# Performance work log

Hardware: AMD Instinct MI355X
Metric: run time of the kernel (lower is better)

## Reference

```python
import jax, jax.numpy as jnp
import numpy as np

EMB = 1024
HEADS = 16
HEADSIZE = EMB // HEADS


def _layernorm(x, gamma, beta, eps=1e-5):
    # LayerNorm over the last dim (headsize), affine.
    mu = jnp.mean(x, axis=-1, keepdims=True)
    var = jnp.var(x, axis=-1, keepdims=True)
    return (x - mu) * jax.lax.rsqrt(var + eps) * gamma + beta


def setup_inputs() -> dict:
    key = jax.random.key(0)
    ks = jax.random.split(key, 12)
    B, TI, TC = 4, 1024, 1024
    s = 1.0 / np.sqrt(EMB)
    inp = {
        "x": jax.random.normal(ks[0], (B, TI, EMB), dtype=jnp.float32),
        "context": jax.random.normal(ks[1], (B, TC, EMB), dtype=jnp.float32),
        # torch nn.Linear weights are (out, in); y = x @ W.T
        "Wq": jax.random.uniform(ks[2], (EMB, EMB), jnp.float32, -s, s),
        "Wk": jax.random.uniform(ks[3], (EMB, EMB), jnp.float32, -s, s),
        "Wv": jax.random.uniform(ks[4], (EMB, EMB), jnp.float32, -s, s),
        "Wu": jax.random.uniform(ks[5], (EMB, EMB), jnp.float32, -s, s),
        "bu": jax.random.uniform(ks[6], (EMB,), jnp.float32, -s, s),
        "q_gamma": jnp.ones((HEADSIZE,), jnp.float32),
        "q_beta": jnp.zeros((HEADSIZE,), jnp.float32),
        "k_gamma": jnp.ones((HEADSIZE,), jnp.float32),
        "k_beta": jnp.zeros((HEADSIZE,), jnp.float32),
    }
    return inp


def reference(x, context, Wq, Wk, Wv, Wu, bu, q_gamma, q_beta, k_gamma, k_beta):
    B, TI, E = x.shape
    TC = context.shape[1]
    T = TI + TC
    xc = jnp.concatenate([x, context], axis=1)  # [B, T, E]

    q = (x @ Wq.T).reshape(B, TI, HEADS, HEADSIZE)
    k = (xc @ Wk.T).reshape(B, T, HEADS, HEADSIZE)
    v = (xc @ Wv.T).reshape(B, T, HEADS, HEADSIZE)

    # optional QK-LayerNorm over headsize
    q = _layernorm(q, q_gamma, q_beta)
    k = _layernorm(k, k_gamma, k_beta)

    scale = E ** 0.25
    q = q / scale
    k = k / scale

    # scores: [B, H, TI, T]
    dot = jnp.einsum("bihd,bjhd->bhij", q, k)
    attn = jax.nn.softmax(dot, axis=-1)
    out = jnp.einsum("bhij,bjhd->bihd", attn, v).reshape(B, TI, E)
    return out @ Wu.T + bu
```

## Files before the change

### kernel.cpp

```cpp
#include <hip/hip_runtime.h>
#include <cstdint>


typedef unsigned short u16;
typedef __attribute__((ext_vector_type(8))) short bf16x8;
typedef __attribute__((ext_vector_type(4))) float f32x4;
typedef __attribute__((ext_vector_type(16))) float f32x16;
typedef __attribute__((ext_vector_type(4))) unsigned short u16x4;
typedef __attribute__((ext_vector_type(2))) unsigned int u32x2;

#define GLDS(gsrc, ldst)                                                              \
  __builtin_amdgcn_global_load_lds(                                                   \
      (const __attribute__((address_space(1))) unsigned int*)(gsrc),                  \
      (__attribute__((address_space(3))) unsigned int*)(ldst), 16, 0, 0)

__device__ __forceinline__ u16 f2bf(float x) {
  unsigned int u = __float_as_uint(x);
  u += 0x7fffu + ((u >> 16) & 1u);
  return (u16)(u >> 16);
}

__device__ __forceinline__ unsigned cvt_pk_bf16(float lo, float hi) {
  unsigned r;
  asm("v_cvt_pk_bf16_f32 %0, %1, %2" : "=v"(r) : "v"(lo), "v"(hi));
  return r;
}

__device__ __forceinline__ f32x4 mfma16(bf16x8 a, bf16x8 b, f32x4 c) {
  return __builtin_amdgcn_mfma_f32_16x16x32_bf16(a, b, c, 0, 0, 0);
}
__device__ __forceinline__ f32x16 mfma32(bf16x8 a, bf16x8 b, f32x16 c) {
  return __builtin_amdgcn_mfma_f32_32x32x16_bf16(a, b, c, 0, 0, 0);
}


__global__ __launch_bounds__(256) void cast_concat(const float* __restrict__ x,
                                                   const float* __restrict__ c,
                                                   u16* __restrict__ o) {
  const int n4 = (8 << 20) / 4;
  for (int i = blockIdx.x * blockDim.x + threadIdx.x; i < n4; i += gridDim.x * blockDim.x) {
    int elem = i * 4;
    int b = elem >> 21;
    int rem = elem & ((1 << 21) - 1);
    int r = rem >> 10;
    int e = rem & 1023;
    const float* src = (r < 1024) ? (x + ((((size_t)(b << 10)) + r) << 10) + e)
                                  : (c + ((((size_t)(b << 10)) + (r - 1024)) << 10) + e);
    float4 v = *(const float4*)src;
    u16x4 ov;
    ov.x = f2bf(v.x); ov.y = f2bf(v.y); ov.z = f2bf(v.z); ov.w = f2bf(v.w);
    *(u16x4*)(o + elem) = ov;
  }
}

__global__ __launch_bounds__(256) void cast_w(const float* __restrict__ w0,
                                              const float* __restrict__ w1,
                                              const float* __restrict__ w2,
                                              const float* __restrict__ w3,
                                              u16* __restrict__ o) {
  const int n4 = (4 << 20) / 4;
  for (int i = blockIdx.x * blockDim.x + threadIdx.x; i < n4; i += gridDim.x * blockDim.x) {
    int elem = i * 4;
    int sel = elem >> 20;
    int loc = elem & ((1 << 20) - 1);
    const float* s = (sel == 0) ? w0 : (sel == 1) ? w1 : (sel == 2) ? w2 : w3;
    float4 v = *(const float4*)(s + loc);
    u16x4 ov;
    ov.x = f2bf(v.x); ov.y = f2bf(v.y); ov.z = f2bf(v.z); ov.w = f2bf(v.w);
    *(u16x4*)(o + elem) = ov;
  }
}


template <int EPI>
__global__ __launch_bounds__(256)
void gemm_bt(const u16* __restrict__ A, const u16* __restrict__ Bw,
             u16* __restrict__ Ob, float* __restrict__ Of,
             const float* __restrict__ P0, const float* __restrict__ P1,
             int M, int N, int K, int rpbo, int rpbi, float oscale) {
  __shared__ alignas(16) u16 lA[2][128 * 32];
  __shared__ alignas(16) u16 lB[2][128 * 32];
  const int tid = threadIdx.x;
  const int wv = tid >> 6, l = tid & 63, g = l >> 4, c16 = l & 15;
  const int wr = wv >> 1, wc = wv & 1;
  const int m0 = blockIdx.x * 128, n0 = blockIdx.y * 128;
  const int arow0 = (m0 / rpbo) * rpbi + (m0 % rpbo);

  f32x4 acc[4][4];
  const f32x4 z4 = {0.f, 0.f, 0.f, 0.f};
#pragma unroll
  for (int i = 0; i < 4; ++i)
#pragma unroll
    for (int j = 0; j < 4; ++j) acc[i][j] = z4;

  const int srow = tid >> 2;
  const int scA = (tid & 3) ^ (srow & 3);
  const u16* aSrc = A + (size_t)(arow0 + srow) * K + scA * 8;
  const u16* bSrc = Bw + (size_t)(n0 + srow) * K + scA * 8;
  char* ldA = (char*)lA;
  char* ldB = (char*)lB;
  const int lof = wv * 1024;

  const int ksteps = K >> 5;
#define STAGE_G(bi, kof)                                   \
  {                                                        \
    char* dA = ldA + (bi)*8192 + lof;                      \
    char* dB = ldB + (bi)*8192 + lof;                      \
    GLDS(aSrc + (kof), dA);                                \
    GLDS(aSrc + (size_t)64 * K + (kof), dA + 4096);        \
    GLDS(bSrc + (kof), dB);                                \
    GLDS(bSrc + (size_t)64 * K + (kof), dB + 4096);        \
  }

  STAGE_G(0, 0);
  __syncthreads();
  int buf = 0;
  for (int kt = 0; kt < ksteps; ++kt) {
    if (kt + 1 < ksteps) STAGE_G(buf ^ 1, (kt + 1) << 5);
    const char* bA = ldA + buf * 8192;
    const char* bB = ldB + buf * 8192;
    bf16x8 af[4], bfr[4];
#pragma unroll
    for (int mi = 0; mi < 4; ++mi) {
      int row = wr * 64 + mi * 16 + c16;
      af[mi] = *(const bf16x8*)(bA + row * 64 + ((g * 16) ^ ((row & 3) << 4)));
    }
#pragma unroll
    for (int ni = 0; ni < 4; ++ni) {
      int row = wc * 64 + ni * 16 + c16;
      bfr[ni] = *(const bf16x8*)(bB + row * 64 + ((g * 16) ^ ((row & 3) << 4)));
    }
#pragma unroll
    for (int mi = 0; mi < 4; ++mi)
#pragma unroll
      for (int ni = 0; ni < 4; ++ni)
        acc[mi][ni] = mfma16(af[mi], bfr[ni], acc[mi][ni]);
    __syncthreads();
    buf ^= 1;
  }
#undef STAGE_G

  if constexpr (EPI == 2) {
#pragma unroll
    for (int ni = 0; ni < 4; ++ni) {
      int col = n0 + wc * 64 + ni * 16 + c16;
      float bv = P0[col];
#pragma unroll
      for (int mi = 0; mi < 4; ++mi) {
        int row = m0 + wr * 64 + mi * 16 + g * 4;
        float* dst = Of + (size_t)row * N + col;
#pragma unroll
        for (int r = 0; r < 4; ++r) dst[(size_t)r * N] = acc[mi][ni][r] + bv;
      }
    }
  } else if constexpr (EPI == 1) {
#pragma unroll
    for (int ni = 0; ni < 4; ++ni) {
      int col = n0 + wc * 64 + ni * 16 + c16;
      int hh = col >> 6, dd = col & 63;
#pragma unroll
      for (int mi = 0; mi < 4; ++mi) {
        int m = m0 + wr * 64 + mi * 16 + g * 4;
        int bb = m >> 11, tt = m & 2047;
        u16x4 o;
#pragma unroll
        for (int r = 0; r < 4; ++r) o[r] = f2bf(acc[mi][ni][r]);
        *(u16x4*)(Ob + ((size_t)((bb * 16 + hh) * 64 + dd)) * 2048 + tt) = o;
      }
    }
  } else {
#pragma unroll
    for (int mi = 0; mi < 4; ++mi) {
      float sum[4], sq[4];
#pragma unroll
      for (int r = 0; r < 4; ++r) {
        float s = 0.f, q = 0.f;
#pragma unroll
        for (int ni = 0; ni < 4; ++ni) {
          float v = acc[mi][ni][r];
          s += v;
          q += v * v;
        }
#pragma unroll
        for (int msk = 1; msk < 16; msk <<= 1) {
          s += __shfl_xor(s, msk);
          q += __shfl_xor(q, msk);
        }
        sum[r] = s;
        sq[r] = q;
      }
#pragma unroll
      for (int ni = 0; ni < 4; ++ni) {
        int dloc = ni * 16 + c16;
        int colg = n0 + wc * 64 + ni * 16 + c16;
        float gv = P0[dloc], bv = P1[dloc];
#pragma unroll
        for (int r = 0; r < 4; ++r) {
          float mean = sum[r] * (1.f / 64.f);
          float var = sq[r] * (1.f / 64.f) - mean * mean;
          float y = (acc[mi][ni][r] - mean) * rsqrtf(var + 1e-5f) * gv + bv;
          int row = m0 + wr * 64 + mi * 16 + g * 4 + r;
          Ob[(size_t)row * N + colg] = f2bf(y * oscale);
        }
      }
    }
  }
}


__global__ __launch_bounds__(512, 4)
void attn_kernel(const u16* __restrict__ Q, const u16* __restrict__ Kb,
                 const u16* __restrict__ Vt, u16* __restrict__ AO) {
  __shared__ alignas(16) u16 lK[2][2][4096];
  __shared__ alignas(16) u16 lV[2][2][4096];
  __shared__ float cmb[4][64][34];
  const int tid = threadIdx.x;
  const int wv = tid >> 6, l = tid & 63;
  const int w4 = wv & 3, kvh2 = wv >> 2;
  const int lq = l & 31, hi = l >> 5;
  const int b = blockIdx.z, h = blockIdx.y, qt = blockIdx.x;
  const int qrow = (b << 10) + (qt << 7) + (w4 << 5) + lq;

  const u16* qp = Q + (size_t)qrow * 1024 + h * 64 + hi * 8;
  bf16x8 qf[4];
#pragma unroll
  for (int kk = 0; kk < 4; ++kk) qf[kk] = *(const bf16x8*)(qp + 16 * kk);

  f32x16 acc[2];
#pragma unroll
  for (int d0 = 0; d0 < 2; ++d0)
#pragma unroll
    for (int i = 0; i < 16; ++i) acc[d0][i] = 0.f;
  float m_run = -1e30f, l_run = 0.f;

  const u16* Ksrc = Kb + ((size_t)(b * 2048) + l) * 1024 + h * 64 + w4 * 8;
  const u16* Vsrc = Vt + ((size_t)((b * 16 + h) * 64) + l) * 2048 + w4 * 8;

#define STAGE_KV(bi, it)                                    \
  {                                                         \
    const int kv0 = ((it) << 7) + (kvh2 << 6);              \
    char* dK = (char*)lK[kvh2][bi] + w4 * 1024;             \
    char* dV = (char*)lV[kvh2][bi] + w4 * 1024;             \
    const u16* ks = Ksrc + (size_t)kv0 * 1024;              \
    const u16* vs = Vsrc + kv0;                             \
    GLDS(ks, dK);                                           \
    GLDS(ks + 32, dK + 4096);                               \
    GLDS(vs, dV);                                           \
    GLDS(vs + 32, dV + 4096);                               \
  }

  STAGE_KV(0, 0);
  __syncthreads();
  int buf = 0;

  for (int it = 0; it < 16; ++it) {
    if (it + 1 < 16) STAGE_KV(buf ^ 1, it + 1);
    const char* bK = (const char*)lK[kvh2][buf];
    const char* bV = (const char*)lV[kvh2][buf];

    f32x16 s[2];
#pragma unroll
    for (int kvh = 0; kvh < 2; ++kvh)
#pragma unroll
      for (int i = 0; i < 16; ++i) s[kvh][i] = 0.f;
    __builtin_amdgcn_s_setprio(1);
#pragma unroll
    for (int kk = 0; kk < 4; ++kk) {
      const char* kbase = bK + (2 * kk + hi) * 1024;
      bf16x8 kf0 = *(const bf16x8*)(kbase + lq * 16);
      bf16x8 kf1 = *(const bf16x8*)(kbase + (32 + lq) * 16);
      s[0] = mfma32(kf0, qf[kk], s[0]);
      s[1] = mfma32(kf1, qf[kk], s[1]);
    }
    __builtin_amdgcn_s_setprio(0);

    float tm0 = fmaxf(s[0][0], s[1][0]), tm1 = fmaxf(s[0][1], s[1][1]);
    float tm2 = fmaxf(s[0][2], s[1][2]), tm3 = fmaxf(s[0][3], s[1][3]);
#pragma unroll
    for (int i = 4; i < 16; i += 4) {
      tm0 = fmaxf(tm0, fmaxf(s[0][i], s[1][i]));
      tm1 = fmaxf(tm1, fmaxf(s[0][i + 1], s[1][i + 1]));
      tm2 = fmaxf(tm2, fmaxf(s[0][i + 2], s[1][i + 2]));
      tm3 = fmaxf(tm3, fmaxf(s[0][i + 3], s[1][i + 3]));
    }
    float tm = fmaxf(fmaxf(tm0, tm1), fmaxf(tm2, tm3));
    tm = fmaxf(tm, __shfl_xor(tm, 32));
    if (!__all(tm <= m_run + 8.f)) {
      float mnew = fmaxf(m_run, tm);
      float corr = __builtin_amdgcn_exp2f(m_run - mnew);
      l_run *= corr;
#pragma unroll
      for (int d0 = 0; d0 < 2; ++d0)
#pragma unroll
        for (int i = 0; i < 16; ++i) acc[d0][i] *= corr;
      m_run = mnew;
    }
    float ts0 = 0.f, ts1 = 0.f, ts2 = 0.f, ts3 = 0.f;
#pragma unroll
    for (int kvh = 0; kvh < 2; ++kvh)
#pragma unroll
      for (int i = 0; i < 16; i += 4) {
        float p0 = __builtin_amdgcn_exp2f(s[kvh][i] - m_run);
        float p1 = __builtin_amdgcn_exp2f(s[kvh][i + 1] - m_run);
        float p2 = __builtin_amdgcn_exp2f(s[kvh][i + 2] - m_run);
        float p3 = __builtin_amdgcn_exp2f(s[kvh][i + 3] - m_run);
        s[kvh][i] = p0; s[kvh][i + 1] = p1; s[kvh][i + 2] = p2; s[kvh][i + 3] = p3;
        ts0 += p0; ts1 += p1; ts2 += p2; ts3 += p3;
      }
    float ts = (ts0 + ts1) + (ts2 + ts3);
    ts += __shfl_xor(ts, 32);
    l_run += ts;

    unsigned int pk[2][4][2];
#pragma unroll
    for (int kvh = 0; kvh < 2; ++kvh)
#pragma unroll
      for (int kp = 0; kp < 4; ++kp)
#pragma unroll
        for (int tt = 0; tt < 2; ++tt)
          pk[kvh][kp][tt] = cvt_pk_bf16(s[kvh][4 * kp + 2 * tt], s[kvh][4 * kp + 2 * tt + 1]);

#pragma unroll
    for (int kk = 0; kk < 4; ++kk) {
      const int kvh = kk >> 1, kb = kk & 1;
      union { unsigned w[4]; bf16x8 v; } bw;
#pragma unroll
      for (int tt = 0; tt < 2; ++tt) {
        unsigned A0 = pk[kvh][2 * kb][tt];
        unsigned A1 = pk[kvh][2 * kb + 1][tt];
        unsigned S = (unsigned)__shfl_xor((int)(hi ? A0 : A1), 32);
        bw.w[tt] = hi ? S : A0;
        bw.w[2 + tt] = hi ? A1 : S;
      }
      const char* vbase = bV + (2 * kk + hi) * 1024;
      bf16x8 vf0 = *(const bf16x8*)(vbase + lq * 16);
      bf16x8 vf1 = *(const bf16x8*)(vbase + (32 + lq) * 16);
      __builtin_amdgcn_s_setprio(1);
      acc[0] = mfma32(vf0, bw.v, acc[0]);
      acc[1] = mfma32(vf1, bw.v, acc[1]);
      __builtin_amdgcn_s_setprio(0);
    }
    __syncthreads();
    buf ^= 1;
  }
#undef STAGE_KV

  if (wv >= 4) {
    float* cp = cmb[w4][l];
#pragma unroll
    for (int d0 = 0; d0 < 2; ++d0)
#pragma unroll
      for (int i = 0; i < 16; ++i) cp[d0 * 16 + i] = acc[d0][i];
    cp[32] = m_run;
    cp[33] = l_run;
  }
  __syncthreads();
  if (wv < 4) {
    const float* cp = cmb[w4][l];
    float m1 = cp[32], l1 = cp[33];
    float mm = fmaxf(m_run, m1);
    float c0 = __builtin_amdgcn_exp2f(m_run - mm);
    float c1 = __builtin_amdgcn_exp2f(m1 - mm);
    float invl = 1.f / (l_run * c0 + l1 * c1);
    float s0 = c0 * invl, s1 = c1 * invl;
#pragma unroll
    for (int d0 = 0; d0 < 2; ++d0)
#pragma unroll
      for (int rg = 0; rg < 4; ++rg) {
        float v0 = acc[d0][4 * rg + 0] * s0 + cp[d0 * 16 + 4 * rg + 0] * s1;
        float v1 = acc[d0][4 * rg + 1] * s0 + cp[d0 * 16 + 4 * rg + 1] * s1;
        float v2 = acc[d0][4 * rg + 2] * s0 + cp[d0 * 16 + 4 * rg + 2] * s1;
        float v3 = acc[d0][4 * rg + 3] * s0 + cp[d0 * 16 + 4 * rg + 3] * s1;
        u32x2 o;
        o.x = cvt_pk_bf16(v0, v1);
        o.y = cvt_pk_bf16(v2, v3);
        int d = 32 * d0 + 8 * rg + 4 * hi;
        *(u32x2*)(AO + (size_t)qrow * 1024 + h * 64 + d) = o;
      }
  }
}


extern "C" void kernel_launch(void* const* d_in, const int* in_sizes, int n_in,
                              void* d_out, int out_size, void* d_ws, size_t ws_size,
                              hipStream_t stream) {
  const float* x = (const float*)d_in[0];
  const float* ctx = (const float*)d_in[1];
  const float* Wq = (const float*)d_in[2];
  const float* Wk = (const float*)d_in[3];
  const float* Wv = (const float*)d_in[4];
  const float* Wu = (const float*)d_in[5];
  const float* bu = (const float*)d_in[6];
  const float* qg = (const float*)d_in[7];
  const float* qb = (const float*)d_in[8];
  const float* kg = (const float*)d_in[9];
  const float* kb = (const float*)d_in[10];
  float* out = (float*)d_out;

  char* w = (char*)d_ws;
  u16* XCB = (u16*)(w);
  u16* WQB = (u16*)(w + ((size_t)16 << 20));
  u16* WKB = (u16*)(w + ((size_t)18 << 20));
  u16* WVB = (u16*)(w + ((size_t)20 << 20));
  u16* WUB = (u16*)(w + ((size_t)22 << 20));
  u16* QBB = (u16*)(w + ((size_t)24 << 20));
  u16* KBB = (u16*)(w + ((size_t)32 << 20));
  u16* VT = (u16*)(w + ((size_t)48 << 20));
  u16* AO = (u16*)(w + ((size_t)64 << 20));

  const float invs = 0.17677669529663687f;
  const float invs_l2e = invs * 1.44269504088896f;

  cast_concat<<<2048, 256, 0, stream>>>(x, ctx, XCB);
  cast_w<<<1024, 256, 0, stream>>>(Wq, Wk, Wv, Wu, WQB);

  gemm_bt<0><<<dim3(32, 8), 256, 0, stream>>>(XCB, WQB, QBB, nullptr, qg, qb,
                                              4096, 1024, 1024, 1024, 2048, invs_l2e);
  gemm_bt<0><<<dim3(64, 8), 256, 0, stream>>>(XCB, WKB, KBB, nullptr, kg, kb,
                                              8192, 1024, 1024, 2048, 2048, invs);
  gemm_bt<1><<<dim3(64, 8), 256, 0, stream>>>(XCB, WVB, VT, nullptr, nullptr, nullptr,
                                              8192, 1024, 1024, 2048, 2048, 1.f);

  attn_kernel<<<dim3(8, 16, 4), 512, 0, stream>>>(QBB, KBB, VT, AO);

  gemm_bt<2><<<dim3(32, 8), 256, 0, stream>>>(AO, WUB, nullptr, out, bu, nullptr,
                                              4096, 1024, 1024, 4096, 4096, 1.f);
}
```

Before: 297.1 us.

## Fuse Q/K/V projections into one launch, retile output GEMM, union attention LDS

The three separate Q, K and V projection GEMM launches become one grid with 24 column-blocks, where blockIdx.y selects the weight and epilogue. Q blocks over context rows exit early. The output projection moves to a dedicated 64x128-tile kernel so more blocks are launched, and MFMA sections get raised wave priority. Attention shared memory now overlaps the K/V buffers with the combine buffer through a union to cut LDS use. These changes aim to remove launch overhead and tail idle time and to improve occupancy. The cost is some idle early-exit blocks and smaller tiles with less reuse in the output GEMM.

```diff
diff --git a/kernel.cpp b/kernel.cpp
--- a/kernel.cpp
+++ b/kernel.cpp
@@ -72,19 +72,25 @@
 }
 
 
-template <int EPI>
 __global__ __launch_bounds__(256)
-void gemm_bt(const u16* __restrict__ A, const u16* __restrict__ Bw,
-             u16* __restrict__ Ob, float* __restrict__ Of,
-             const float* __restrict__ P0, const float* __restrict__ P1,
-             int M, int N, int K, int rpbo, int rpbi, float oscale) {
+void gemm_qkv(const u16* __restrict__ XCB, const u16* __restrict__ Wall,
+              u16* __restrict__ QBB, u16* __restrict__ KBB, u16* __restrict__ VT,
+              const float* __restrict__ qg, const float* __restrict__ qb,
+              const float* __restrict__ kg, const float* __restrict__ kb,
+              float sQ, float sK) {
+  const int ny = blockIdx.y;
+  const int which = ny >> 3;
+  const int m0 = blockIdx.x << 7;
+  if (which == 0 && (m0 & 2047) >= 1024) return;
+  const int n0 = (ny & 7) << 7;
+  const u16* Bw = Wall + ((size_t)which << 20);
+  const int K = 1024, N = 1024;
+
   __shared__ alignas(16) u16 lA[2][128 * 32];
   __shared__ alignas(16) u16 lB[2][128 * 32];
   const int tid = threadIdx.x;
   const int wv = tid >> 6, l = tid & 63, g = l >> 4, c16 = l & 15;
   const int wr = wv >> 1, wc = wv & 1;
-  const int m0 = blockIdx.x * 128, n0 = blockIdx.y * 128;
-  const int arow0 = (m0 / rpbo) * rpbi + (m0 % rpbo);
 
   f32x4 acc[4][4];
   const f32x4 z4 = {0.f, 0.f, 0.f, 0.f};
@@ -95,13 +101,12 @@
 
   const int srow = tid >> 2;
   const int scA = (tid & 3) ^ (srow & 3);
-  const u16* aSrc = A + (size_t)(arow0 + srow) * K + scA * 8;
+  const u16* aSrc = XCB + (size_t)(m0 + srow) * K + scA * 8;
   const u16* bSrc = Bw + (size_t)(n0 + srow) * K + scA * 8;
   char* ldA = (char*)lA;
   char* ldB = (char*)lB;
   const int lof = wv * 1024;
 
-  const int ksteps = K >> 5;
 #define STAGE_G(bi, kof)                                   \
   {                                                        \
     char* dA = ldA + (bi)*8192 + lof;                      \
@@ -115,8 +120,8 @@
   STAGE_G(0, 0);
   __syncthreads();
   int buf = 0;
-  for (int kt = 0; kt < ksteps; ++kt) {
-    if (kt + 1 < ksteps) STAGE_G(buf ^ 1, (kt + 1) << 5);
+  for (int kt = 0; kt < 32; ++kt) {
+    if (kt + 1 < 32) STAGE_G(buf ^ 1, (kt + 1) << 5);
     const char* bA = ldA + buf * 8192;
     const char* bB = ldB + buf * 8192;
     bf16x8 af[4], bfr[4];
@@ -130,30 +135,19 @@
       int row = wc * 64 + ni * 16 + c16;
       bfr[ni] = *(const bf16x8*)(bB + row * 64 + ((g * 16) ^ ((row & 3) << 4)));
     }
+    __builtin_amdgcn_s_setprio(1);
 #pragma unroll
     for (int mi = 0; mi < 4; ++mi)
 #pragma unroll
       for (int ni = 0; ni < 4; ++ni)
         acc[mi][ni] = mfma16(af[mi], bfr[ni], acc[mi][ni]);
+    __builtin_amdgcn_s_setprio(0);
     __syncthreads();
     buf ^= 1;
   }
 #undef STAGE_G
 
-  if constexpr (EPI == 2) {
-#pragma unroll
-    for (int ni = 0; ni < 4; ++ni) {
-      int col = n0 + wc * 64 + ni * 16 + c16;
-      float bv = P0[col];
-#pragma unroll
-      for (int mi = 0; mi < 4; ++mi) {
-        int row = m0 + wr * 64 + mi * 16 + g * 4;
-        float* dst = Of + (size_t)row * N + col;
-#pragma unroll
-        for (int r = 0; r < 4; ++r) dst[(size_t)r * N] = acc[mi][ni][r] + bv;
-      }
-    }
-  } else if constexpr (EPI == 1) {
+  if (which == 2) {
 #pragma unroll
     for (int ni = 0; ni < 4; ++ni) {
       int col = n0 + wc * 64 + ni * 16 + c16;
@@ -165,10 +159,14 @@
         u16x4 o;
 #pragma unroll
         for (int r = 0; r < 4; ++r) o[r] = f2bf(acc[mi][ni][r]);
-        *(u16x4*)(Ob + ((size_t)((bb * 16 + hh) * 64 + dd)) * 2048 + tt) = o;
+        *(u16x4*)(VT + ((size_t)((bb * 16 + hh) * 64 + dd)) * 2048 + tt) = o;
       }
     }
   } else {
+    const float* G = which ? kg : qg;
+    const float* Bt = which ? kb : qb;
+    const float osc = which ? sK : sQ;
+    u16* Ob = which ? KBB : QBB;
 #pragma unroll
     for (int mi = 0; mi < 4; ++mi) {
       float sum[4], sq[4];
@@ -193,16 +191,97 @@
       for (int ni = 0; ni < 4; ++ni) {
         int dloc = ni * 16 + c16;
         int colg = n0 + wc * 64 + ni * 16 + c16;
-        float gv = P0[dloc], bv = P1[dloc];
+        float gv = G[dloc], bv = Bt[dloc];
 #pragma unroll
         for (int r = 0; r < 4; ++r) {
           float mean = sum[r] * (1.f / 64.f);
           float var = sq[r] * (1.f / 64.f) - mean * mean;
           float y = (acc[mi][ni][r] - mean) * rsqrtf(var + 1e-5f) * gv + bv;
           int row = m0 + wr * 64 + mi * 16 + g * 4 + r;
-          Ob[(size_t)row * N + colg] = f2bf(y * oscale);
+          int orow = which ? row : (((row >> 11) << 10) | (row & 1023));
+          Ob[(size_t)orow * N + colg] = f2bf(y * osc);
         }
       }
+    }
+  }
+}
+
+
+__global__ __launch_bounds__(256)
+void gemm_u64(const u16* __restrict__ A, const u16* __restrict__ Bw,
+              float* __restrict__ Of, const float* __restrict__ bias) {
+  const int K = 1024, N = 1024;
+  __shared__ alignas(16) u16 lA[2][64 * 32];
+  __shared__ alignas(16) u16 lB[2][128 * 32];
+  const int tid = threadIdx.x;
+  const int wv = tid >> 6, l = tid & 63, g = l >> 4, c16 = l & 15;
+  const int wr = wv >> 1, wc = wv & 1;
+  const int m0 = blockIdx.x << 6, n0 = blockIdx.y << 7;
+
+  f32x4 acc[2][4];
+  const f32x4 z4 = {0.f, 0.f, 0.f, 0.f};
+#pragma unroll
+  for (int i = 0; i < 2; ++i)
+#pragma unroll
+    for (int j = 0; j < 4; ++j) acc[i][j] = z4;
+
+  const int srow = tid >> 2;
+  const int sc = (tid & 3) ^ (srow & 3);
+  const u16* aSrc = A + (size_t)(m0 + srow) * K + sc * 8;
+  const u16* bSrc = Bw + (size_t)(n0 + srow) * K + sc * 8;
+  char* ldA = (char*)lA;
+  char* ldB = (char*)lB;
+  const int lof = wv * 1024;
+
+#define STAGE_U(bi, kof)                                   \
+  {                                                        \
+    char* dA = ldA + (bi)*4096 + lof;                      \
+    char* dB = ldB + (bi)*8192 + lof;                      \
+    GLDS(aSrc + (kof), dA);                                \
+    GLDS(bSrc + (kof), dB);                                \
+    GLDS(bSrc + (size_t)64 * K + (kof), dB + 4096);        \
+  }
+
+  STAGE_U(0, 0);
+  __syncthreads();
+  int buf = 0;
+  for (int kt = 0; kt < 32; ++kt) {
+    if (kt + 1 < 32) STAGE_U(buf ^ 1, (kt + 1) << 5);
+    const char* bA = ldA + buf * 4096;
+    const char* bB = ldB + buf * 8192;
+    bf16x8 af[2], bfr[4];
+#pragma unroll
+    for (int mi = 0; mi < 2; ++mi) {
+      int row = wr * 32 + mi * 16 + c16;
+      af[mi] = *(const bf16x8*)(bA + row * 64 + ((g * 16) ^ ((row & 3) << 4)));
+    }
+#pragma unroll
+    for (int ni = 0; ni < 4; ++ni) {
+      int row = wc * 64 + ni * 16 + c16;
+      bfr[ni] = *(const bf16x8*)(bB + row * 64 + ((g * 16) ^ ((row & 3) << 4)));
+    }
+    __builtin_amdgcn_s_setprio(1);
+#pragma unroll
+    for (int mi = 0; mi < 2; ++mi)
+#pragma unroll
+      for (int ni = 0; ni < 4; ++ni)
+        acc[mi][ni] = mfma16(af[mi], bfr[ni], acc[mi][ni]);
+    __builtin_amdgcn_s_setprio(0);
+    __syncthreads();
+    buf ^= 1;
+  }
+#undef STAGE_U
+
+#pragma unroll
+  for (int ni = 0; ni < 4; ++ni) {
+    int col = n0 + wc * 64 + ni * 16 + c16;
+    float bv = bias[col];
+#pragma unroll
+    for (int mi = 0; mi < 2; ++mi) {
+      int row = m0 + wr * 32 + mi * 16 + g * 4;
+      float* dst = Of + (size_t)row * N + col;
+#pragma unroll
+      for (int r = 0; r < 4; ++r) dst[(size_t)r * N] = acc[mi][ni][r] + bv;
     }
   }
 }
@@ -211,9 +290,10 @@
 __global__ __launch_bounds__(512, 4)
 void attn_kernel(const u16* __restrict__ Q, const u16* __restrict__ Kb,
                  const u16* __restrict__ Vt, u16* __restrict__ AO) {
-  __shared__ alignas(16) u16 lK[2][2][4096];
-  __shared__ alignas(16) u16 lV[2][2][4096];
-  __shared__ float cmb[4][64][34];
+  __shared__ union alignas(16) {
+    struct { u16 K[2][2][4096]; u16 V[2][2][4096]; } kv;
+    float cmb[4][64][34];
+  } sm;
   const int tid = threadIdx.x;
   const int wv = tid >> 6, l = tid & 63;
   const int w4 = wv & 3, kvh2 = wv >> 2;
@@ -239,8 +319,8 @@
 #define STAGE_KV(bi, it)                                    \
   {                                                         \
     const int kv0 = ((it) << 7) + (kvh2 << 6);              \
-    char* dK = (char*)lK[kvh2][bi] + w4 * 1024;             \
-    char* dV = (char*)lV[kvh2][bi] + w4 * 1024;             \
+    char* dK = (char*)sm.kv.K[kvh2][bi] + w4 * 1024;        \
+    char* dV = (char*)sm.kv.V[kvh2][bi] + w4 * 1024;        \
     const u16* ks = Ksrc + (size_t)kv0 * 1024;              \
     const u16* vs = Vsrc + kv0;                             \
     GLDS(ks, dK);                                           \
@@ -255,8 +335,8 @@
 
   for (int it = 0; it < 16; ++it) {
     if (it + 1 < 16) STAGE_KV(buf ^ 1, it + 1);
-    const char* bK = (const char*)lK[kvh2][buf];
-    const char* bV = (const char*)lV[kvh2][buf];
+    const char* bK = (const char*)sm.kv.K[kvh2][buf];
+    const char* bV = (const char*)sm.kv.V[kvh2][buf];
 
     f32x16 s[2];
 #pragma unroll
@@ -320,6 +400,7 @@
         for (int tt = 0; tt < 2; ++tt)
           pk[kvh][kp][tt] = cvt_pk_bf16(s[kvh][4 * kp + 2 * tt], s[kvh][4 * kp + 2 * tt + 1]);
 
+    __builtin_amdgcn_s_setprio(1);
 #pragma unroll
     for (int kk = 0; kk < 4; ++kk) {
       const int kvh = kk >> 1, kb = kk & 1;
@@ -335,18 +416,17 @@
       const char* vbase = bV + (2 * kk + hi) * 1024;
       bf16x8 vf0 = *(const bf16x8*)(vbase + lq * 16);
       bf16x8 vf1 = *(const bf16x8*)(vbase + (32 + lq) * 16);
-      __builtin_amdgcn_s_setprio(1);
       acc[0] = mfma32(vf0, bw.v, acc[0]);
       acc[1] = mfma32(vf1, bw.v, acc[1]);
-      __builtin_amdgcn_s_setprio(0);
-    }
+    }
+    __builtin_amdgcn_s_setprio(0);
     __syncthreads();
     buf ^= 1;
   }
 #undef STAGE_KV
 
   if (wv >= 4) {
-    float* cp = cmb[w4][l];
+    float* cp = sm.cmb[w4][l];
 #pragma unroll
     for (int d0 = 0; d0 < 2; ++d0)
 #pragma unroll
@@ -356,7 +436,7 @@
   }
   __syncthreads();
   if (wv < 4) {
-    const float* cp = cmb[w4][l];
+    const float* cp = sm.cmb[w4][l];
     float m1 = cp[32], l1 = cp[33];
     float mm = fmaxf(m_run, m1);
     float c0 = __builtin_amdgcn_exp2f(m_run - mm);
@@ -400,9 +480,6 @@
   char* w = (char*)d_ws;
   u16* XCB = (u16*)(w);
   u16* WQB = (u16*)(w + ((size_t)16 << 20));
-  u16* WKB = (u16*)(w + ((size_t)18 << 20));
-  u16* WVB = (u16*)(w + ((size_t)20 << 20));
-  u16* WUB = (u16*)(w + ((size_t)22 << 20));
   u16* QBB = (u16*)(w + ((size_t)24 << 20));
   u16* KBB = (u16*)(w + ((size_t)32 << 20));
   u16* VT = (u16*)(w + ((size_t)48 << 20));
@@ -414,15 +491,10 @@
   cast_concat<<<2048, 256, 0, stream>>>(x, ctx, XCB);
   cast_w<<<1024, 256, 0, stream>>>(Wq, Wk, Wv, Wu, WQB);
 
-  gemm_bt<0><<<dim3(32, 8), 256, 0, stream>>>(XCB, WQB, QBB, nullptr, qg, qb,
-                                              4096, 1024, 1024, 1024, 2048, invs_l2e);
-  gemm_bt<0><<<dim3(64, 8), 256, 0, stream>>>(XCB, WKB, KBB, nullptr, kg, kb,
-                                              8192, 1024, 1024, 2048, 2048, invs);
-  gemm_bt<1><<<dim3(64, 8), 256, 0, stream>>>(XCB, WVB, VT, nullptr, nullptr, nullptr,
-                                              8192, 1024, 1024, 2048, 2048, 1.f);
+  gemm_qkv<<<dim3(64, 24), 256, 0, stream>>>(XCB, WQB, QBB, KBB, VT,
+                                             qg, qb, kg, kb, invs_l2e, invs);
 
   attn_kernel<<<dim3(8, 16, 4), 512, 0, stream>>>(QBB, KBB, VT, AO);
 
-  gemm_bt<2><<<dim3(32, 8), 256, 0, stream>>>(AO, WUB, nullptr, out, bu, nullptr,
-                                              4096, 1024, 1024, 4096, 4096, 1.f);
-}
+  gemm_u64<<<dim3(64, 8), 256, 0, stream>>>(AO, WQB + ((size_t)3 << 20), out, bu);
+}
```

Result: faster. 276.5 us (-6.9%).
